# Kernel tuning notes

Measured on AMD Instinct MI355X. Metric: run time of the kernel, lower is better.

Reference implementation:

```python
import jax, jax.numpy as jnp
import numpy as np

H = 32  # hidden size per direction (hard-wired in module)


def _gru_scan(x_proj, W_hh, b_hh, reverse):
    """x_proj: [T, B, 3H] = x @ W_ih.T + b_ih (precomputed). Returns all hidden states [T, B, H].
    Gate order follows PyTorch: (r, z, n)."""
    def step(h, xp):
        gh = h @ W_hh.T + b_hh                      # [B, 3H]
        xr, xz, xn = jnp.split(xp, 3, axis=-1)
        hr, hz, hn = jnp.split(gh, 3, axis=-1)
        r = jax.nn.sigmoid(xr + hr)
        z = jax.nn.sigmoid(xz + hz)
        n = jnp.tanh(xn + r * hn)
        h_new = (1.0 - z) * n + z * h
        return h_new, h_new

    B = x_proj.shape[1]
    h0 = jnp.zeros((B, H), x_proj.dtype)
    _, ys = jax.lax.scan(step, h0, x_proj, reverse=reverse)
    return ys  # ys[t] = hidden after consuming x[t] (fwd) or x[T-1..t] (bwd)


def setup_inputs() -> dict:
    key = jax.random.key(0)
    ks = jax.random.split(key, 14)
    B, T = 2048, 512
    s_ih = 1.0 / np.sqrt(H)
    inp = {
        "x": jax.random.normal(ks[0], (B, T, 1), dtype=jnp.float32),
        # forward-direction GRU params (PyTorch layout: [3H, in], [3H, H], [3H])
        "W_ih_f": jax.random.uniform(ks[1], (3 * H, 1), jnp.float32, -s_ih, s_ih),
        "W_hh_f": jax.random.uniform(ks[2], (3 * H, H), jnp.float32, -s_ih, s_ih),
        "b_ih_f": jax.random.uniform(ks[3], (3 * H,), jnp.float32, -s_ih, s_ih),
        "b_hh_f": jax.random.uniform(ks[4], (3 * H,), jnp.float32, -s_ih, s_ih),
        # backward-direction GRU params
        "W_ih_b": jax.random.uniform(ks[5], (3 * H, 1), jnp.float32, -s_ih, s_ih),
        "W_hh_b": jax.random.uniform(ks[6], (3 * H, H), jnp.float32, -s_ih, s_ih),
        "b_ih_b": jax.random.uniform(ks[7], (3 * H,), jnp.float32, -s_ih, s_ih),
        "b_hh_b": jax.random.uniform(ks[8], (3 * H,), jnp.float32, -s_ih, s_ih),
        # MLP head: Linear(64,16) -> ReLU -> Linear(16,1) -> Sigmoid
        "W1": jax.random.uniform(ks[9], (16, 2 * H), jnp.float32, -0.125, 0.125),
        "b1": jax.random.uniform(ks[10], (16,), jnp.float32, -0.125, 0.125),
        "W2": jax.random.uniform(ks[11], (1, 16), jnp.float32, -0.25, 0.25),
        "b2": jax.random.uniform(ks[12], (1,), jnp.float32, -0.25, 0.25),
    }
    return inp


def reference(x, W_ih_f, W_hh_f, b_ih_f, b_hh_f,
              W_ih_b, W_hh_b, b_ih_b, b_hh_b,
              W1, b1, W2, b2):
    xt = jnp.swapaxes(x, 0, 1)                 # [T, B, 1]
    # Precompute input projections for all timesteps (input_size=1 so this is cheap)
    xpf = xt @ W_ih_f.T + b_ih_f               # [T, B, 3H]
    xpb = xt @ W_ih_b.T + b_ih_b               # [T, B, 3H]
    ys_f = _gru_scan(xpf, W_hh_f, b_hh_f, reverse=False)
    ys_b = _gru_scan(xpb, W_hh_b, b_hh_b, reverse=True)
    # out[:, -1, :] in torch = concat(fwd hidden at t=T-1, bwd hidden at t=T-1)
    out_last = jnp.concatenate([ys_f[-1], ys_b[-1]], axis=-1)   # [B, 64]
    h1 = jax.nn.relu(out_last @ W1.T + b1)                      # [B, 16]
    return jax.nn.sigmoid(h1 @ W2.T + b2)                       # [B, 1]
```

## Files before the change

kernel.cpp:

```cpp
#include <hip/hip_runtime.h>


typedef float vf2 __attribute__((ext_vector_type(2)));
typedef float vf4 __attribute__((ext_vector_type(4)));
typedef _Float16 f16;
typedef f16 h2 __attribute__((ext_vector_type(2)));
typedef f16 h8 __attribute__((ext_vector_type(8)));

#define TT 512
#define HH 32

#define PIN(v) asm volatile("" : "+v"(v))

#define LOG2E 1.44269504f

__device__ __forceinline__ float fast_sigm(float a) {
  return __builtin_amdgcn_rcpf(1.0f + __builtin_amdgcn_exp2f(-LOG2E * a));
}
__device__ __forceinline__ float fast_tanh(float a) {
  return __builtin_fmaf(-2.0f,
      __builtin_amdgcn_rcpf(1.0f + __builtin_amdgcn_exp2f(2.0f * LOG2E * a)),
      1.0f);
}

__device__ __forceinline__ h2 pack_h2(vf2 a, float s) {
  h2 r = {(f16)(a.x * s), (f16)(a.y * s)};
  return r;
}

#define LDW16(P, BASE, S) \
  h2 P##0=pack_h2(Wp[(BASE)+0],(S)),  P##1=pack_h2(Wp[(BASE)+1],(S)), \
     P##2=pack_h2(Wp[(BASE)+2],(S)),  P##3=pack_h2(Wp[(BASE)+3],(S)), \
     P##4=pack_h2(Wp[(BASE)+4],(S)),  P##5=pack_h2(Wp[(BASE)+5],(S)), \
     P##6=pack_h2(Wp[(BASE)+6],(S)),  P##7=pack_h2(Wp[(BASE)+7],(S)), \
     P##8=pack_h2(Wp[(BASE)+8],(S)),  P##9=pack_h2(Wp[(BASE)+9],(S)), \
     P##A=pack_h2(Wp[(BASE)+10],(S)), P##B=pack_h2(Wp[(BASE)+11],(S)), \
     P##C=pack_h2(Wp[(BASE)+12],(S)), P##D=pack_h2(Wp[(BASE)+13],(S)), \
     P##E=pack_h2(Wp[(BASE)+14],(S)), P##F=pack_h2(Wp[(BASE)+15],(S)); \
  PIN(P##0);PIN(P##1);PIN(P##2);PIN(P##3);PIN(P##4);PIN(P##5);PIN(P##6);PIN(P##7); \
  PIN(P##8);PIN(P##9);PIN(P##A);PIN(P##B);PIN(P##C);PIN(P##D);PIN(P##E);PIN(P##F)

#define FDOT16(A0, A1, P, SEED) \
  float A0 = __builtin_amdgcn_fdot2(q0, P##0, (SEED), false); \
  float A1 = __builtin_amdgcn_fdot2(q1, P##1, 0.0f, false); \
  A0 = __builtin_amdgcn_fdot2(q2, P##2, A0, false);  A1 = __builtin_amdgcn_fdot2(q3, P##3, A1, false); \
  A0 = __builtin_amdgcn_fdot2(q4, P##4, A0, false);  A1 = __builtin_amdgcn_fdot2(q5, P##5, A1, false); \
  A0 = __builtin_amdgcn_fdot2(q6, P##6, A0, false);  A1 = __builtin_amdgcn_fdot2(q7, P##7, A1, false); \
  A0 = __builtin_amdgcn_fdot2(q8, P##8, A0, false);  A1 = __builtin_amdgcn_fdot2(q9, P##9, A1, false); \
  A0 = __builtin_amdgcn_fdot2(qA, P##A, A0, false);  A1 = __builtin_amdgcn_fdot2(qB, P##B, A1, false); \
  A0 = __builtin_amdgcn_fdot2(qC, P##C, A0, false);  A1 = __builtin_amdgcn_fdot2(qD, P##D, A1, false); \
  A0 = __builtin_amdgcn_fdot2(qE, P##E, A0, false);  A1 = __builtin_amdgcn_fdot2(qF, P##F, A1, false)

__global__ __launch_bounds__(256)
__attribute__((amdgpu_waves_per_eu(1, 1)))
void gru_bidir_head(const float* __restrict__ X,
                    const float* __restrict__ Wih_f, const float* __restrict__ Whh_f,
                    const float* __restrict__ bih_f, const float* __restrict__ bhh_f,
                    const float* __restrict__ Wih_b,
                    const float* __restrict__ bih_b, const float* __restrict__ bhh_b,
                    const float* __restrict__ W1, const float* __restrict__ b1,
                    const float* __restrict__ W2, const float* __restrict__ b2,
                    float* __restrict__ out)
{
  __shared__ float xbuf[8][TT];
  __shared__ f16   hbuf[8][HH];
  __shared__ float obuf[8][64];

  const int g  = threadIdx.x & 31;
  const int rs = threadIdx.x >> 5;
  const int b  = (blockIdx.x << 3) + rs;

  const vf4* Xr4 = (const vf4*)(X + (size_t)b * TT);
  vf4* xb4 = (vf4*)&xbuf[rs][0];
  #pragma unroll
  for (int q = 0; q < 4; ++q) xb4[g + 32 * q] = Xr4[g + 32 * q];

  const vf2* Wp = (const vf2*)Whh_f;
  const float s1 = -LOG2E;
  const float s2 = 2.0f * LOG2E;
  LDW16(Wr, (g)        * 16, s1);
  LDW16(Wz, (HH + g)   * 16, s1);
  LDW16(Wn, (2*HH + g) * 16, s2);

  float xwr = Wih_f[g] * s1, xwz = Wih_f[HH + g] * s1, xwn = Wih_f[2*HH + g] * s2;
  float cbr = (bih_f[g]      + bhh_f[g])      * s1;
  float cbz = (bih_f[HH + g] + bhh_f[HH + g]) * s1;
  float cbn = bih_f[2*HH + g] * s2;
  float cbh = bhh_f[2*HH + g] * s2;
  PIN(xwr); PIN(xwz); PIN(xwn); PIN(cbr); PIN(cbz); PIN(cbn); PIN(cbh);

  float h = 0.0f;
  hbuf[rs][g] = (f16)0.0f;
  __builtin_amdgcn_wave_barrier();

  const h8*  hv = (const h8*)&hbuf[rs][0];
  const vf4* xv = (const vf4*)&xbuf[rs][0];
  vf4 x4 = xv[0];

  #pragma unroll 1
  for (int tg = 0; tg < TT / 4; ++tg) {
    const vf4 x4n = xv[tg + 1 < TT / 4 ? tg + 1 : tg];

    float sr0 = __builtin_fmaf(x4.x, xwr, cbr), sz0 = __builtin_fmaf(x4.x, xwz, cbz),
          sn0 = __builtin_fmaf(x4.x, xwn, cbn);
    float sr1 = __builtin_fmaf(x4.y, xwr, cbr), sz1 = __builtin_fmaf(x4.y, xwz, cbz),
          sn1 = __builtin_fmaf(x4.y, xwn, cbn);
    float sr2 = __builtin_fmaf(x4.z, xwr, cbr), sz2 = __builtin_fmaf(x4.z, xwz, cbz),
          sn2 = __builtin_fmaf(x4.z, xwn, cbn);
    float sr3 = __builtin_fmaf(x4.w, xwr, cbr), sz3 = __builtin_fmaf(x4.w, xwz, cbz),
          sn3 = __builtin_fmaf(x4.w, xwn, cbn);

    #pragma unroll
    for (int u = 0; u < 4; ++u) {
      const float sr = (u == 0) ? sr0 : (u == 1) ? sr1 : (u == 2) ? sr2 : sr3;
      const float sz = (u == 0) ? sz0 : (u == 1) ? sz1 : (u == 2) ? sz2 : sz3;
      const float sn = (u == 0) ? sn0 : (u == 1) ? sn1 : (u == 2) ? sn2 : sn3;

      const h8 H0 = hv[0], H1 = hv[1], H2 = hv[2], H3 = hv[3];
      const h2 q0 = {H0[0], H0[1]}, q1 = {H0[2], H0[3]}, q2 = {H0[4], H0[5]}, q3 = {H0[6], H0[7]},
               q4 = {H1[0], H1[1]}, q5 = {H1[2], H1[3]}, q6 = {H1[4], H1[5]}, q7 = {H1[6], H1[7]},
               q8 = {H2[0], H2[1]}, q9 = {H2[2], H2[3]}, qA = {H2[4], H2[5]}, qB = {H2[6], H2[7]},
               qC = {H3[0], H3[1]}, qD = {H3[2], H3[3]}, qE = {H3[4], H3[5]}, qF = {H3[6], H3[7]};

      FDOT16(Ra, Rb, Wr, sr);
      FDOT16(Za, Zb, Wz, sz);
      FDOT16(Na, Nb, Wn, cbh);

      const float ar = Ra + Rb;
      const float az = Za + Zb;
      const float r = __builtin_amdgcn_rcpf(1.0f + __builtin_amdgcn_exp2f(ar));
      const float z = __builtin_amdgcn_rcpf(1.0f + __builtin_amdgcn_exp2f(az));
      const float y = __builtin_fmaf(r, Na + Nb, sn);
      const float n = __builtin_fmaf(-2.0f,
          __builtin_amdgcn_rcpf(1.0f + __builtin_amdgcn_exp2f(y)), 1.0f);
      h = __builtin_fmaf(z, h - n, n);

      hbuf[rs][g] = (f16)h;
      __builtin_amdgcn_wave_barrier();
    }
    x4 = x4n;
  }

  const float xl  = xbuf[rs][TT - 1];
  const float rb  = fast_sigm(__builtin_fmaf(xl, Wih_b[g],      bih_b[g]      + bhh_b[g]));
  const float zb  = fast_sigm(__builtin_fmaf(xl, Wih_b[HH + g], bih_b[HH + g] + bhh_b[HH + g]));
  const float xnb = __builtin_fmaf(xl, Wih_b[2*HH + g], bih_b[2*HH + g]);
  const float nb  = fast_tanh(__builtin_fmaf(rb, bhh_b[2*HH + g], xnb));
  const float hb  = nb - zb * nb;

  obuf[rs][g]      = h;
  obuf[rs][32 + g] = hb;
  __builtin_amdgcn_wave_barrier();

  const int j = g & 15;
  const vf4* W1r = (const vf4*)(W1 + j * 64);
  const vf4* hc  = (const vf4*)&obuf[rs][0];
  vf4 a4 = W1r[0] * hc[0];
  #pragma unroll
  for (int q = 1; q < 16; ++q)
    a4 = __builtin_elementwise_fma(W1r[q], hc[q], a4);
  float acc = b1[j] + (a4.x + a4.y) + (a4.z + a4.w);
  float h1 = fmaxf(acc, 0.0f) * W2[j];
  h1 += __shfl_down(h1, 8, 16);
  h1 += __shfl_down(h1, 4, 16);
  h1 += __shfl_down(h1, 2, 16);
  h1 += __shfl_down(h1, 1, 16);
  if (g == 0) out[b] = fast_sigm(h1 + b2[0]);
}

extern "C" void kernel_launch(void* const* d_in, const int* in_sizes, int n_in,
                              void* d_out, int out_size, void* d_ws, size_t ws_size,
                              hipStream_t stream) {
  const float* X     = (const float*)d_in[0];
  const float* Wih_f = (const float*)d_in[1];
  const float* Whh_f = (const float*)d_in[2];
  const float* bih_f = (const float*)d_in[3];
  const float* bhh_f = (const float*)d_in[4];
  const float* Wih_b = (const float*)d_in[5];
  const float* bih_b = (const float*)d_in[7];
  const float* bhh_b = (const float*)d_in[8];
  const float* W1    = (const float*)d_in[9];
  const float* b1    = (const float*)d_in[10];
  const float* W2    = (const float*)d_in[11];
  const float* b2    = (const float*)d_in[12];
  float* out = (float*)d_out;

  gru_bidir_head<<<256, 256, 0, stream>>>(X, Wih_f, Whh_f, bih_f, bhh_f,
                                          Wih_b, bih_b, bhh_b, W1, b1, W2, b2, out);
}
```

Baseline: 176.0 us.

## Broadcast GRU hidden state via DPP and swizzle instead of LDS

```diff
diff --git a/kernel.cpp b/kernel.cpp
--- a/kernel.cpp
+++ b/kernel.cpp
@@ -5,7 +5,6 @@
 typedef float vf4 __attribute__((ext_vector_type(4)));
 typedef _Float16 f16;
 typedef f16 h2 __attribute__((ext_vector_type(2)));
-typedef f16 h8 __attribute__((ext_vector_type(8)));
 
 #define TT 512
 #define HH 32
@@ -23,33 +22,47 @@
       1.0f);
 }
 
-__device__ __forceinline__ h2 pack_h2(vf2 a, float s) {
-  h2 r = {(f16)(a.x * s), (f16)(a.y * s)};
+template <int CTRL>
+__device__ __forceinline__ int dpp(int v) {
+  return __builtin_amdgcn_mov_dpp(v, CTRL, 0xF, 0xF, true);
+}
+#define DPP_X1 0xB1
+#define DPP_X2 0x4E
+#define DPP_HM 0x141
+#define DPP_M  0x140
+#define SWZ_X16 0x401F
+
+__device__ __forceinline__ h2 asH2(int v) { return __builtin_bit_cast(h2, v); }
+__device__ __forceinline__ int asI(h2 v) { return __builtin_bit_cast(int, v); }
+
+__device__ __forceinline__ h2 wpair(const float* Wrow, int g, int e0, int e1,
+                                    float s) {
+  h2 r = {(f16)(Wrow[g ^ e0] * s), (f16)(Wrow[g ^ e1] * s)};
   return r;
 }
 
-#define LDW16(P, BASE, S) \
-  h2 P##0=pack_h2(Wp[(BASE)+0],(S)),  P##1=pack_h2(Wp[(BASE)+1],(S)), \
-     P##2=pack_h2(Wp[(BASE)+2],(S)),  P##3=pack_h2(Wp[(BASE)+3],(S)), \
-     P##4=pack_h2(Wp[(BASE)+4],(S)),  P##5=pack_h2(Wp[(BASE)+5],(S)), \
-     P##6=pack_h2(Wp[(BASE)+6],(S)),  P##7=pack_h2(Wp[(BASE)+7],(S)), \
-     P##8=pack_h2(Wp[(BASE)+8],(S)),  P##9=pack_h2(Wp[(BASE)+9],(S)), \
-     P##A=pack_h2(Wp[(BASE)+10],(S)), P##B=pack_h2(Wp[(BASE)+11],(S)), \
-     P##C=pack_h2(Wp[(BASE)+12],(S)), P##D=pack_h2(Wp[(BASE)+13],(S)), \
-     P##E=pack_h2(Wp[(BASE)+14],(S)), P##F=pack_h2(Wp[(BASE)+15],(S)); \
+#define LDWG(P, ROWPTR, S) \
+  h2 P##0 = wpair(ROWPTR, g, 0, 1, S),   P##1 = wpair(ROWPTR, g, 2, 3, S), \
+     P##2 = wpair(ROWPTR, g, 7, 6, S),   P##3 = wpair(ROWPTR, g, 5, 4, S), \
+     P##4 = wpair(ROWPTR, g, 15, 14, S), P##5 = wpair(ROWPTR, g, 13, 12, S), \
+     P##6 = wpair(ROWPTR, g, 8, 9, S),   P##7 = wpair(ROWPTR, g, 10, 11, S), \
+     P##8 = wpair(ROWPTR, g, 16, 17, S), P##9 = wpair(ROWPTR, g, 18, 19, S), \
+     P##A = wpair(ROWPTR, g, 23, 22, S), P##B = wpair(ROWPTR, g, 21, 20, S), \
+     P##C = wpair(ROWPTR, g, 31, 30, S), P##D = wpair(ROWPTR, g, 29, 28, S), \
+     P##E = wpair(ROWPTR, g, 24, 25, S), P##F = wpair(ROWPTR, g, 26, 27, S); \
   PIN(P##0);PIN(P##1);PIN(P##2);PIN(P##3);PIN(P##4);PIN(P##5);PIN(P##6);PIN(P##7); \
   PIN(P##8);PIN(P##9);PIN(P##A);PIN(P##B);PIN(P##C);PIN(P##D);PIN(P##E);PIN(P##F)
 
 #define FDOT16(A0, A1, P, SEED) \
-  float A0 = __builtin_amdgcn_fdot2(q0, P##0, (SEED), false); \
-  float A1 = __builtin_amdgcn_fdot2(q1, P##1, 0.0f, false); \
-  A0 = __builtin_amdgcn_fdot2(q2, P##2, A0, false);  A1 = __builtin_amdgcn_fdot2(q3, P##3, A1, false); \
-  A0 = __builtin_amdgcn_fdot2(q4, P##4, A0, false);  A1 = __builtin_amdgcn_fdot2(q5, P##5, A1, false); \
-  A0 = __builtin_amdgcn_fdot2(q6, P##6, A0, false);  A1 = __builtin_amdgcn_fdot2(q7, P##7, A1, false); \
-  A0 = __builtin_amdgcn_fdot2(q8, P##8, A0, false);  A1 = __builtin_amdgcn_fdot2(q9, P##9, A1, false); \
-  A0 = __builtin_amdgcn_fdot2(qA, P##A, A0, false);  A1 = __builtin_amdgcn_fdot2(qB, P##B, A1, false); \
-  A0 = __builtin_amdgcn_fdot2(qC, P##C, A0, false);  A1 = __builtin_amdgcn_fdot2(qD, P##D, A1, false); \
-  A0 = __builtin_amdgcn_fdot2(qE, P##E, A0, false);  A1 = __builtin_amdgcn_fdot2(qF, P##F, A1, false)
+  float A0 = __builtin_amdgcn_fdot2(y0, P##0, (SEED), false); \
+  float A1 = __builtin_amdgcn_fdot2(y1, P##1, 0.0f, false); \
+  A0 = __builtin_amdgcn_fdot2(y2, P##2, A0, false);  A1 = __builtin_amdgcn_fdot2(y3, P##3, A1, false); \
+  A0 = __builtin_amdgcn_fdot2(y4, P##4, A0, false);  A1 = __builtin_amdgcn_fdot2(y5, P##5, A1, false); \
+  A0 = __builtin_amdgcn_fdot2(y6, P##6, A0, false);  A1 = __builtin_amdgcn_fdot2(y7, P##7, A1, false); \
+  A0 = __builtin_amdgcn_fdot2(y8, P##8, A0, false);  A1 = __builtin_amdgcn_fdot2(y9, P##9, A1, false); \
+  A0 = __builtin_amdgcn_fdot2(yA, P##A, A0, false);  A1 = __builtin_amdgcn_fdot2(yB, P##B, A1, false); \
+  A0 = __builtin_amdgcn_fdot2(yC, P##C, A0, false);  A1 = __builtin_amdgcn_fdot2(yD, P##D, A1, false); \
+  A0 = __builtin_amdgcn_fdot2(yE, P##E, A0, false);  A1 = __builtin_amdgcn_fdot2(yF, P##F, A1, false)
 
 __global__ __launch_bounds__(256)
 __attribute__((amdgpu_waves_per_eu(1, 1)))
@@ -63,7 +76,6 @@
                     float* __restrict__ out)
 {
   __shared__ float xbuf[8][TT];
-  __shared__ f16   hbuf[8][HH];
   __shared__ float obuf[8][64];
 
   const int g  = threadIdx.x & 31;
@@ -74,13 +86,16 @@
   vf4* xb4 = (vf4*)&xbuf[rs][0];
   #pragma unroll
   for (int q = 0; q < 4; ++q) xb4[g + 32 * q] = Xr4[g + 32 * q];
-
-  const vf2* Wp = (const vf2*)Whh_f;
+  __builtin_amdgcn_wave_barrier();
+
   const float s1 = -LOG2E;
   const float s2 = 2.0f * LOG2E;
-  LDW16(Wr, (g)        * 16, s1);
-  LDW16(Wz, (HH + g)   * 16, s1);
-  LDW16(Wn, (2*HH + g) * 16, s2);
+  const float* Wr_row = Whh_f + (size_t)(g)        * HH;
+  const float* Wz_row = Whh_f + (size_t)(HH + g)   * HH;
+  const float* Wn_row = Whh_f + (size_t)(2*HH + g) * HH;
+  LDWG(Wr, Wr_row, s1);
+  LDWG(Wz, Wz_row, s1);
+  LDWG(Wn, Wn_row, s2);
 
   float xwr = Wih_f[g] * s1, xwz = Wih_f[HH + g] * s1, xwn = Wih_f[2*HH + g] * s2;
   float cbr = (bih_f[g]      + bhh_f[g])      * s1;
@@ -90,10 +105,6 @@
   PIN(xwr); PIN(xwz); PIN(xwn); PIN(cbr); PIN(cbz); PIN(cbn); PIN(cbh);
 
   float h = 0.0f;
-  hbuf[rs][g] = (f16)0.0f;
-  __builtin_amdgcn_wave_barrier();
-
-  const h8*  hv = (const h8*)&hbuf[rs][0];
   const vf4* xv = (const vf4*)&xbuf[rs][0];
   vf4 x4 = xv[0];
 
@@ -116,11 +127,31 @@
       const float sz = (u == 0) ? sz0 : (u == 1) ? sz1 : (u == 2) ? sz2 : sz3;
       const float sn = (u == 0) ? sn0 : (u == 1) ? sn1 : (u == 2) ? sn2 : sn3;
 
-      const h8 H0 = hv[0], H1 = hv[1], H2 = hv[2], H3 = hv[3];
-      const h2 q0 = {H0[0], H0[1]}, q1 = {H0[2], H0[3]}, q2 = {H0[4], H0[5]}, q3 = {H0[6], H0[7]},
-               q4 = {H1[0], H1[1]}, q5 = {H1[2], H1[3]}, q6 = {H1[4], H1[5]}, q7 = {H1[6], H1[7]},
-               q8 = {H2[0], H2[1]}, q9 = {H2[2], H2[3]}, qA = {H2[4], H2[5]}, qB = {H2[6], H2[7]},
-               qC = {H3[0], H3[1]}, qD = {H3[2], H3[3]}, qE = {H3[4], H3[5]}, qF = {H3[6], H3[7]};
+      const f16 hf = (f16)h;
+      const h2 self = {hf, hf};
+      const int nb  = dpp<DPP_X1>(asI(self));
+      const h2 pair = {self[0], asH2(nb)[0]};
+      const int p0 = asI(pair);
+      const int p1 = dpp<DPP_X2>(p0);
+      const int p2 = dpp<DPP_HM>(p0);
+      const int p3 = dpp<DPP_HM>(p1);
+      const int p4 = dpp<DPP_M>(p0);
+      const int p5 = dpp<DPP_M>(p1);
+      const int p6 = dpp<DPP_M>(p2);
+      const int p7 = dpp<DPP_M>(p3);
+      const int q8 = __builtin_amdgcn_ds_swizzle(p0, SWZ_X16);
+      const int q9 = __builtin_amdgcn_ds_swizzle(p1, SWZ_X16);
+      const int qA = __builtin_amdgcn_ds_swizzle(p2, SWZ_X16);
+      const int qB = __builtin_amdgcn_ds_swizzle(p3, SWZ_X16);
+      const int qC = __builtin_amdgcn_ds_swizzle(p4, SWZ_X16);
+      const int qD = __builtin_amdgcn_ds_swizzle(p5, SWZ_X16);
+      const int qE = __builtin_amdgcn_ds_swizzle(p6, SWZ_X16);
+      const int qF = __builtin_amdgcn_ds_swizzle(p7, SWZ_X16);
+
+      const h2 y0 = asH2(p0), y1 = asH2(p1), y2 = asH2(p2), y3 = asH2(p3),
+               y4 = asH2(p4), y5 = asH2(p5), y6 = asH2(p6), y7 = asH2(p7),
+               y8 = asH2(q8), y9 = asH2(q9), yA = asH2(qA), yB = asH2(qB),
+               yC = asH2(qC), yD = asH2(qD), yE = asH2(qE), yF = asH2(qF);
 
       FDOT16(Ra, Rb, Wr, sr);
       FDOT16(Za, Zb, Wz, sz);
@@ -134,9 +165,6 @@
       const float n = __builtin_fmaf(-2.0f,
           __builtin_amdgcn_rcpf(1.0f + __builtin_amdgcn_exp2f(y)), 1.0f);
       h = __builtin_fmaf(z, h - n, n);
-
-      hbuf[rs][g] = (f16)h;
-      __builtin_amdgcn_wave_barrier();
     }
     x4 = x4n;
   }
@@ -145,8 +173,8 @@
   const float rb  = fast_sigm(__builtin_fmaf(xl, Wih_b[g],      bih_b[g]      + bhh_b[g]));
   const float zb  = fast_sigm(__builtin_fmaf(xl, Wih_b[HH + g], bih_b[HH + g] + bhh_b[HH + g]));
   const float xnb = __builtin_fmaf(xl, Wih_b[2*HH + g], bih_b[2*HH + g]);
-  const float nb  = fast_tanh(__builtin_fmaf(rb, bhh_b[2*HH + g], xnb));
-  const float hb  = nb - zb * nb;
+  const float nb_ = fast_tanh(__builtin_fmaf(rb, bhh_b[2*HH + g], xnb));
+  const float hb  = nb_ - zb * nb_;
 
   obuf[rs][g]      = h;
   obuf[rs][32 + g] = hb;
```

Result: slower. 188.9 us (+7.3%).
